# Kernel tuning notes

Measured on AMD Instinct MI355X. Metric: run time of the kernel, lower is better.

The kernel has to match this reference:

```python
import jax, jax.numpy as jnp
import numpy as np


def setup_inputs() -> dict:
    key = jax.random.key(0)
    k1, k2, k3 = jax.random.split(key, 3)
    B, C, H, W = 64, 512, 28, 28
    K = 32
    std = 1.0 / (K * C) ** 0.5
    x = jax.random.normal(k1, (B, C, H, W), dtype=jnp.float32)
    codewords = jax.random.uniform(k2, (K, C), dtype=jnp.float32, minval=-std, maxval=std)
    scale = jax.random.uniform(k3, (K,), dtype=jnp.float32, minval=-1.0, maxval=0.0)
    return {"x": x, "codewords": codewords, "scale": scale}


def reference(x, codewords, scale):
    # x: (B, C, H, W) -> descriptors (B, N, C)
    B, C, H, W = x.shape
    K = codewords.shape[0]
    xd = x.reshape(B, C, H * W).transpose(0, 2, 1)  # (B, N, C)

    # scaled L2: scale_k * ||x_n - c_k||^2, expanded without (B,N,K,C) intermediate
    x_sq = jnp.sum(xd * xd, axis=-1, keepdims=True)            # (B, N, 1)
    c_sq = jnp.sum(codewords * codewords, axis=-1)             # (K,)
    xc = jnp.einsum("bnc,kc->bnk", xd, codewords)              # (B, N, K)
    dist = scale * (x_sq - 2.0 * xc + c_sq)                    # (B, N, K)

    A = jax.nn.softmax(dist, axis=2)                           # (B, N, K)

    # encoded_k = sum_n A[b,n,k] * (x[b,n] - c[k])
    wx = jnp.einsum("bnk,bnc->bkc", A, xd)                     # (B, K, C)
    wsum = jnp.sum(A, axis=1)                                  # (B, K)
    encoded = wx - wsum[:, :, None] * codewords[None, :, :]    # (B, K, C)
    return encoded
```

## Files before the change

kernel.cpp:

```cpp
#include <hip/hip_runtime.h>

#define BB 64
#define CC 512
#define NPIX 784
#define KK 32
#define NSA 13
#define AS 800
#define CW_S 520
#define NSTEP 24

typedef __attribute__((ext_vector_type(8))) short short8;
typedef __attribute__((ext_vector_type(4))) float floatx4;
typedef __attribute__((ext_vector_type(4))) unsigned short ushort4v;

#define WSUM_OFF (BB * KK * AS)

__device__ __forceinline__ unsigned short f2bf(float f) {
    union { float f; unsigned u; } v; v.f = f;
    return (unsigned short)((v.u + 0x7FFFu + ((v.u >> 16) & 1u)) >> 16);
}
__device__ __forceinline__ float bf2f(unsigned short h) {
    union { unsigned u; float f; } v; v.u = ((unsigned)h) << 16; return v.f;
}
__device__ __forceinline__ short8 pack8(const float4& a, const float4& b) {
    short8 r;
    r[0] = (short)f2bf(a.x); r[1] = (short)f2bf(a.y);
    r[2] = (short)f2bf(a.z); r[3] = (short)f2bf(a.w);
    r[4] = (short)f2bf(b.x); r[5] = (short)f2bf(b.y);
    r[6] = (short)f2bf(b.z); r[7] = (short)f2bf(b.w);
    return r;
}

__global__ __launch_bounds__(256, 4) void kA(const float* __restrict__ x,
                                             const float* __restrict__ cw,
                                             const float* __restrict__ scale,
                                             unsigned short* __restrict__ Ag)
{
    __shared__ __align__(16) unsigned short cs[KK * CW_S];
    __shared__ float csq_p[8][KK];
    __shared__ float csq_l[KK];
    __shared__ float wredA[4][KK];

    const int t    = threadIdx.x;
    const int lane = t & 63, w = t >> 6;
    const int col  = lane & 15, quad = lane >> 4;
    const int split = blockIdx.x, b = blockIdx.y;
    const int p0    = (split < 12) ? split * 64 : 720;

    if (split == 0 && t < 64) {
        const short8 z = {0, 0, 0, 0, 0, 0, 0, 0};
        const int k = t >> 1, off = (t & 1) * 8;
        *(short8*)&Ag[(size_t)b * KK * AS + (size_t)k * AS + NPIX + off] = z;
    }

#pragma unroll 4
    for (int j = 0; j < 16; ++j) {
        const int qidx = t + j * 256;
        const int row = qidx >> 7, qc = qidx & 127;
        const float4 v = *(const float4*)&cw[row * CC + qc * 4];
        ushort4v p; p.x = f2bf(v.x); p.y = f2bf(v.y); p.z = f2bf(v.z); p.w = f2bf(v.w);
        *(ushort4v*)&cs[row * CW_S + qc * 4] = p;
    }
    __syncthreads();
    {
        const int k = t & 31, part = t >> 5;
        float s = 0.f;
        for (int i = 0; i < 64; ++i) {
            const float v = bf2f(cs[k * CW_S + part * 64 + i]);
            s += v * v;
        }
        csq_p[part][k] = s;
    }
    __syncthreads();
    if (t < KK) {
        float s = 0.f;
#pragma unroll
        for (int p = 0; p < 8; ++p) s += csq_p[p][t];
        csq_l[t] = s;
    }
    __syncthreads();

    const float s0 = scale[col], s1 = scale[col + 16];
    const float q0 = csq_l[col], q1 = csq_l[col + 16];

    const int px = p0 + w * 16 + col;
    const float* xb = x + (size_t)b * CC * NPIX + px;

    floatx4 acc0 = {0.f, 0.f, 0.f, 0.f};
    floatx4 acc1 = {0.f, 0.f, 0.f, 0.f};
    float xsqp = 0.f;
    float buf[3][8];

#pragma unroll
    for (int j = 0; j < 8; ++j) buf[0][j] = xb[(size_t)(0 * 32 + quad * 8 + j) * NPIX];
#pragma unroll
    for (int j = 0; j < 8; ++j) buf[1][j] = xb[(size_t)(1 * 32 + quad * 8 + j) * NPIX];

#pragma unroll
    for (int kc = 0; kc < 16; ++kc) {
        const int cur = kc % 3;
        if (kc + 2 < 16) {
            const int nb = (kc + 2) % 3;
            const int cb = (kc + 2) * 32 + quad * 8;
#pragma unroll
            for (int j = 0; j < 8; ++j) buf[nb][j] = xb[(size_t)(cb + j) * NPIX];
        }
        short8 a;
#pragma unroll
        for (int j = 0; j < 8; ++j) {
            const float v = buf[cur][j];
            xsqp += v * v;
            a[j] = (short)f2bf(v);
        }
        const int cb0 = kc * 32 + quad * 8;
        const short8 b0 = *(const short8*)&cs[col * CW_S + cb0];
        const short8 b1 = *(const short8*)&cs[(col + 16) * CW_S + cb0];
        acc0 = __builtin_amdgcn_mfma_f32_16x16x32_bf16(a, b0, acc0, 0, 0, 0);
        acc1 = __builtin_amdgcn_mfma_f32_16x16x32_bf16(a, b1, acc1, 0, 0, 0);
    }

    xsqp += __shfl_xor(xsqp, 16);
    xsqp += __shfl_xor(xsqp, 32);

    unsigned short* Ab = Ag + (size_t)b * KK * AS + p0 + w * 16;
    float ts0 = 0.f, ts1 = 0.f;
#pragma unroll
    for (int r = 0; r < 4; ++r) {
        const float xq = __shfl(xsqp, quad * 4 + r);
        const float d0 = s0 * (xq + q0 - 2.f * acc0[r]);
        const float d1 = s1 * (xq + q1 - 2.f * acc1[r]);
        float mx = fmaxf(d0, d1);
        mx = fmaxf(mx, __shfl_xor(mx, 1));
        mx = fmaxf(mx, __shfl_xor(mx, 2));
        mx = fmaxf(mx, __shfl_xor(mx, 4));
        mx = fmaxf(mx, __shfl_xor(mx, 8));
        const float e0 = __expf(d0 - mx), e1 = __expf(d1 - mx);
        float sm = e0 + e1;
        sm += __shfl_xor(sm, 1);
        sm += __shfl_xor(sm, 2);
        sm += __shfl_xor(sm, 4);
        sm += __shfl_xor(sm, 8);
        const float inv = 1.f / sm;
        const float a0 = e0 * inv, a1 = e1 * inv;
        Ab[col * AS + quad * 4 + r]        = f2bf(a0);
        Ab[(col + 16) * AS + quad * 4 + r] = f2bf(a1);
        ts0 += a0; ts1 += a1;
    }

    ts0 += __shfl_xor(ts0, 16); ts0 += __shfl_xor(ts0, 32);
    ts1 += __shfl_xor(ts1, 16); ts1 += __shfl_xor(ts1, 32);
    if (quad == 0) { wredA[w][col] = ts0; wredA[w][col + 16] = ts1; }
    __syncthreads();
    if (t < KK) {
        float s;
        if (split < 12) s = wredA[0][t] + wredA[1][t] + wredA[2][t] + wredA[3][t];
        else            s = wredA[3][t];
        float* wsf = (float*)(Ag + WSUM_OFF);
        wsf[(size_t)(split * BB + b) * KK + t] = s;
    }
}

__global__ __launch_bounds__(256) void kB(const float* __restrict__ x,
                                          const float* __restrict__ cw,
                                          const unsigned short* __restrict__ Ag,
                                          float* __restrict__ out)
{
    __shared__ float wsum_l[KK];

    const int t    = threadIdx.x;
    const int lane = t & 63, w = t >> 6;
    const int col  = lane & 15, quad = lane >> 4;
    const int cch  = blockIdx.x, b = blockIdx.y;

    const unsigned short* Ab = Ag + (size_t)b * KK * AS;

    if (t < KK) {
        const float* wsf = (const float*)(Ag + WSUM_OFF);
        float s = 0.f;
#pragma unroll
        for (int sp = 0; sp < NSA; ++sp) s += wsf[(size_t)(sp * BB + b) * KK + t];
        wsum_l[t] = s;
    }

    const int c = cch * 64 + w * 16 + col;
    const float* xp = x + ((size_t)b * CC + c) * NPIX;
    const unsigned short* a0p = Ab + (size_t)col * AS;
    const unsigned short* a1p = Ab + (size_t)(col + 16) * AS;
    const int qo = quad * 8;

    floatx4 acc0 = {0.f, 0.f, 0.f, 0.f};
    floatx4 acc1 = {0.f, 0.f, 0.f, 0.f};
#pragma unroll 6
    for (int s = 0; s < NSTEP; ++s) {
        const int off = s * 32 + qo;
        const short8 av0 = *(const short8*)&a0p[off];
        const short8 av1 = *(const short8*)&a1p[off];
        const float4 xv0 = *(const float4*)&xp[off];
        const float4 xv1 = *(const float4*)&xp[off + 4];
        const short8 bv = pack8(xv0, xv1);
        acc0 = __builtin_amdgcn_mfma_f32_16x16x32_bf16(av0, bv, acc0, 0, 0, 0);
        acc1 = __builtin_amdgcn_mfma_f32_16x16x32_bf16(av1, bv, acc1, 0, 0, 0);
    }
    {
        const int off = NSTEP * 32 + qo;
        const short8 av0 = *(const short8*)&a0p[off];
        const short8 av1 = *(const short8*)&a1p[off];
        float4 xv0 = make_float4(0.f, 0.f, 0.f, 0.f);
        float4 xv1 = make_float4(0.f, 0.f, 0.f, 0.f);
        if (quad < 2) {
            xv0 = *(const float4*)&xp[off];
            xv1 = *(const float4*)&xp[off + 4];
        }
        const short8 bv = pack8(xv0, xv1);
        acc0 = __builtin_amdgcn_mfma_f32_16x16x32_bf16(av0, bv, acc0, 0, 0, 0);
        acc1 = __builtin_amdgcn_mfma_f32_16x16x32_bf16(av1, bv, acc1, 0, 0, 0);
    }

    __syncthreads();

    float* ob = out + (size_t)b * KK * CC + c;
    const float* cp = cw + c;
#pragma unroll
    for (int r = 0; r < 4; ++r) {
        const int k0 = quad * 4 + r;
        ob[(size_t)k0 * CC]        = acc0[r] - wsum_l[k0]      * cp[(size_t)k0 * CC];
        ob[(size_t)(k0 + 16) * CC] = acc1[r] - wsum_l[k0 + 16] * cp[(size_t)(k0 + 16) * CC];
    }
}

extern "C" void kernel_launch(void* const* d_in, const int* in_sizes, int n_in,
                              void* d_out, int out_size, void* d_ws, size_t ws_size,
                              hipStream_t stream) {
    const float* x     = (const float*)d_in[0];
    const float* cw    = (const float*)d_in[1];
    const float* scale = (const float*)d_in[2];
    float* out = (float*)d_out;
    unsigned short* Ag = (unsigned short*)d_ws;

    kA<<<dim3(NSA, BB), dim3(256), 0, stream>>>(x, cw, scale, Ag);
    kB<<<dim3(8, BB), dim3(256), 0, stream>>>(x, cw, Ag, out);
}
```

Measured before the change: 183.4 us.

## Stream x tiles into LDS via global_load_lds double buffering in kA

Replaces the register triple-buffered x loads in kA with direct global-to-LDS asynchronous loads (global_load_lds), double-buffered per wave with explicit vmcnt waits, so more loads stay in flight while the MFMAs run. LDS use grows by 32 KB per block and launch_bounds occupancy drops from 4 to 2 blocks per CU. The intent is to hide global latency better. The cost is lower occupancy and manual waitcnt scheduling that depends on the exact count of outstanding loads.

```diff
diff --git a/kernel.cpp b/kernel.cpp
--- a/kernel.cpp
+++ b/kernel.cpp
@@ -31,12 +31,28 @@
     return r;
 }
 
-__global__ __launch_bounds__(256, 4) void kA(const float* __restrict__ x,
+#define GLOAD_LDS(gp, lp)                                                       \
+    __builtin_amdgcn_global_load_lds(                                           \
+        (const __attribute__((address_space(1))) unsigned int*)(const void*)(gp), \
+        (__attribute__((address_space(3))) unsigned int*)(void*)(lp), 4, 0, 0)
+
+#define ISSUEG(g, bf) {                                                         \
+    _Pragma("unroll")                                                           \
+    for (int _kl = 0; _kl < 2; ++_kl) {                                         \
+        _Pragma("unroll")                                                       \
+        for (int _j = 0; _j < 8; ++_j) {                                        \
+            const float* _src = xb + (size_t)((g) * 64 + _kl * 32 + quad * 8 + _j) * NPIX; \
+            GLOAD_LDS(_src, &gbuf[w][bf][(_kl * 8 + _j) * 64]);                 \
+        }                                                                       \
+    } }
+
+__global__ __launch_bounds__(256, 2) void kA(const float* __restrict__ x,
                                              const float* __restrict__ cw,
                                              const float* __restrict__ scale,
                                              unsigned short* __restrict__ Ag)
 {
     __shared__ __align__(16) unsigned short cs[KK * CW_S];
+    __shared__ __align__(16) float gbuf[4][2][1024];
     __shared__ float csq_p[8][KK];
     __shared__ float csq_l[KK];
     __shared__ float wredA[4][KK];
@@ -89,34 +105,32 @@
     floatx4 acc0 = {0.f, 0.f, 0.f, 0.f};
     floatx4 acc1 = {0.f, 0.f, 0.f, 0.f};
     float xsqp = 0.f;
-    float buf[3][8];
-
-#pragma unroll
-    for (int j = 0; j < 8; ++j) buf[0][j] = xb[(size_t)(0 * 32 + quad * 8 + j) * NPIX];
-#pragma unroll
-    for (int j = 0; j < 8; ++j) buf[1][j] = xb[(size_t)(1 * 32 + quad * 8 + j) * NPIX];
-
-#pragma unroll
-    for (int kc = 0; kc < 16; ++kc) {
-        const int cur = kc % 3;
-        if (kc + 2 < 16) {
-            const int nb = (kc + 2) % 3;
-            const int cb = (kc + 2) * 32 + quad * 8;
-#pragma unroll
-            for (int j = 0; j < 8; ++j) buf[nb][j] = xb[(size_t)(cb + j) * NPIX];
-        }
-        short8 a;
-#pragma unroll
-        for (int j = 0; j < 8; ++j) {
-            const float v = buf[cur][j];
-            xsqp += v * v;
-            a[j] = (short)f2bf(v);
-        }
-        const int cb0 = kc * 32 + quad * 8;
-        const short8 b0 = *(const short8*)&cs[col * CW_S + cb0];
-        const short8 b1 = *(const short8*)&cs[(col + 16) * CW_S + cb0];
-        acc0 = __builtin_amdgcn_mfma_f32_16x16x32_bf16(a, b0, acc0, 0, 0, 0);
-        acc1 = __builtin_amdgcn_mfma_f32_16x16x32_bf16(a, b1, acc1, 0, 0, 0);
+
+    ISSUEG(0, 0);
+#pragma unroll
+    for (int g = 0; g < 8; ++g) {
+        if (g < 7) {
+            ISSUEG(g + 1, (g + 1) & 1);
+            asm volatile("s_waitcnt vmcnt(16)" ::: "memory");
+        } else {
+            asm volatile("s_waitcnt vmcnt(0)" ::: "memory");
+        }
+        __builtin_amdgcn_sched_barrier(0);
+#pragma unroll
+        for (int kl = 0; kl < 2; ++kl) {
+            const int kc = g * 2 + kl;
+            float va[8];
+#pragma unroll
+            for (int j = 0; j < 8; ++j) va[j] = gbuf[w][g & 1][(kl * 8 + j) * 64 + lane];
+            short8 a;
+#pragma unroll
+            for (int j = 0; j < 8; ++j) { xsqp += va[j] * va[j]; a[j] = (short)f2bf(va[j]); }
+            const int cb = kc * 32 + quad * 8;
+            const short8 b0 = *(const short8*)&cs[col * CW_S + cb];
+            const short8 b1 = *(const short8*)&cs[(col + 16) * CW_S + cb];
+            acc0 = __builtin_amdgcn_mfma_f32_16x16x32_bf16(a, b0, acc0, 0, 0, 0);
+            acc1 = __builtin_amdgcn_mfma_f32_16x16x32_bf16(a, b1, acc1, 0, 0, 0);
+        }
     }
 
     xsqp += __shfl_xor(xsqp, 16);
```

After: 182.2 us. No clear change (-0.6%).

## Precompute bf16 codewords once and stage x tile in LDS for kA

Applied to the files above, without the earlier changes.

Adds a one-block prep kernel that converts codewords to bf16 and computes their squared norms once into workspace, so each kA block no longer redoes this. kA now loads its 64-pixel x tile with coalesced float4 reads into a padded bf16 LDS buffer, computes x squared norms there, and reads MFMA operands from LDS. Codeword operands come straight from global/L2. The cost is an extra kernel launch and a large LDS footprint (about 66KB), which lowers occupancy (launch bounds reduced to 2).

```diff
diff --git a/kernel.cpp b/kernel.cpp
--- a/kernel.cpp
+++ b/kernel.cpp
@@ -6,7 +6,7 @@
 #define KK 32
 #define NSA 13
 #define AS 800
-#define CW_S 520
+#define XS_S 66
 #define NSTEP 24
 
 typedef __attribute__((ext_vector_type(8))) short short8;
@@ -14,13 +14,12 @@
 typedef __attribute__((ext_vector_type(4))) unsigned short ushort4v;
 
 #define WSUM_OFF (BB * KK * AS)
+#define CWB_OFF  (WSUM_OFF + 2 * NSA * BB * KK)
+#define CSQ_OFF  (CWB_OFF + KK * CC)
 
 __device__ __forceinline__ unsigned short f2bf(float f) {
     union { float f; unsigned u; } v; v.f = f;
     return (unsigned short)((v.u + 0x7FFFu + ((v.u >> 16) & 1u)) >> 16);
-}
-__device__ __forceinline__ float bf2f(unsigned short h) {
-    union { unsigned u; float f; } v; v.u = ((unsigned)h) << 16; return v.f;
 }
 __device__ __forceinline__ short8 pack8(const float4& a, const float4& b) {
     short8 r;
@@ -31,14 +30,39 @@
     return r;
 }
 
-__global__ __launch_bounds__(256, 4) void kA(const float* __restrict__ x,
-                                             const float* __restrict__ cw,
+__global__ __launch_bounds__(256) void kPrep(const float* __restrict__ cw,
+                                             unsigned short* __restrict__ Ag)
+{
+    __shared__ float red[KK][8];
+    const int t = threadIdx.x;
+    const int k = t >> 3, part = t & 7;
+    unsigned short* cwb = Ag + CWB_OFF;
+    float* csqg = (float*)(Ag + CSQ_OFF);
+    const float* cp = cw + k * CC + part * 64;
+    float s = 0.f;
+#pragma unroll 16
+    for (int i = 0; i < 64; ++i) {
+        const float v = cp[i];
+        s += v * v;
+        cwb[k * CC + part * 64 + i] = f2bf(v);
+    }
+    red[k][part] = s;
+    __syncthreads();
+    if (t < KK) {
+        float ss = 0.f;
+#pragma unroll
+        for (int p = 0; p < 8; ++p) ss += red[t][p];
+        csqg[t] = ss;
+    }
+}
+
+__global__ __launch_bounds__(256, 2) void kA(const float* __restrict__ x,
                                              const float* __restrict__ scale,
                                              unsigned short* __restrict__ Ag)
 {
-    __shared__ __align__(16) unsigned short cs[KK * CW_S];
-    __shared__ float csq_p[8][KK];
-    __shared__ float csq_l[KK];
+    __shared__ __align__(16) unsigned short xs[CC * XS_S];
+    __shared__ float xsq_p[16][64];
+    __shared__ float xsq_l[64];
     __shared__ float wredA[4][KK];
 
     const int t    = threadIdx.x;
@@ -53,80 +77,66 @@
         *(short8*)&Ag[(size_t)b * KK * AS + (size_t)k * AS + NPIX + off] = z;
     }
 
-#pragma unroll 4
-    for (int j = 0; j < 16; ++j) {
-        const int qidx = t + j * 256;
-        const int row = qidx >> 7, qc = qidx & 127;
-        const float4 v = *(const float4*)&cw[row * CC + qc * 4];
-        ushort4v p; p.x = f2bf(v.x); p.y = f2bf(v.y); p.z = f2bf(v.z); p.w = f2bf(v.w);
-        *(ushort4v*)&cs[row * CW_S + qc * 4] = p;
-    }
-    __syncthreads();
-    {
-        const int k = t & 31, part = t >> 5;
+    const float* xb = x + (size_t)b * CC * NPIX + p0;
+    const int csub = t >> 4;
+    const int pg   = t & 15;
+    float sx0 = 0.f, sx1 = 0.f, sx2 = 0.f, sx3 = 0.f;
+#pragma unroll
+    for (int g = 0; g < 4; ++g) {
+        float4 v[8];
+#pragma unroll
+        for (int i = 0; i < 8; ++i) {
+            const int c = (g * 8 + i) * 16 + csub;
+            v[i] = *(const float4*)&xb[(size_t)c * NPIX + pg * 4];
+        }
+#pragma unroll
+        for (int i = 0; i < 8; ++i) {
+            const int c = (g * 8 + i) * 16 + csub;
+            sx0 += v[i].x * v[i].x; sx1 += v[i].y * v[i].y;
+            sx2 += v[i].z * v[i].z; sx3 += v[i].w * v[i].w;
+            ushort4v p; p.x = f2bf(v[i].x); p.y = f2bf(v[i].y);
+            p.z = f2bf(v[i].z); p.w = f2bf(v[i].w);
+            *(ushort4v*)&xs[c * XS_S + pg * 4] = p;
+        }
+    }
+    xsq_p[csub][pg * 4 + 0] = sx0;
+    xsq_p[csub][pg * 4 + 1] = sx1;
+    xsq_p[csub][pg * 4 + 2] = sx2;
+    xsq_p[csub][pg * 4 + 3] = sx3;
+    __syncthreads();
+    if (t < 64) {
         float s = 0.f;
-        for (int i = 0; i < 64; ++i) {
-            const float v = bf2f(cs[k * CW_S + part * 64 + i]);
-            s += v * v;
-        }
-        csq_p[part][k] = s;
-    }
-    __syncthreads();
-    if (t < KK) {
-        float s = 0.f;
-#pragma unroll
-        for (int p = 0; p < 8; ++p) s += csq_p[p][t];
-        csq_l[t] = s;
-    }
-    __syncthreads();
-
+#pragma unroll
+        for (int r = 0; r < 16; ++r) s += xsq_p[r][t];
+        xsq_l[t] = s;
+    }
+    __syncthreads();
+
+    const unsigned short* cwb = Ag + CWB_OFF;
+    const float* csqg = (const float*)(Ag + CSQ_OFF);
     const float s0 = scale[col], s1 = scale[col + 16];
-    const float q0 = csq_l[col], q1 = csq_l[col + 16];
-
-    const int px = p0 + w * 16 + col;
-    const float* xb = x + (size_t)b * CC * NPIX + px;
+    const float q0 = csqg[col], q1 = csqg[col + 16];
+    const int wpx = w * 16 + col;
 
     floatx4 acc0 = {0.f, 0.f, 0.f, 0.f};
     floatx4 acc1 = {0.f, 0.f, 0.f, 0.f};
-    float xsqp = 0.f;
-    float buf[3][8];
-
-#pragma unroll
-    for (int j = 0; j < 8; ++j) buf[0][j] = xb[(size_t)(0 * 32 + quad * 8 + j) * NPIX];
-#pragma unroll
-    for (int j = 0; j < 8; ++j) buf[1][j] = xb[(size_t)(1 * 32 + quad * 8 + j) * NPIX];
-
 #pragma unroll
     for (int kc = 0; kc < 16; ++kc) {
-        const int cur = kc % 3;
-        if (kc + 2 < 16) {
-            const int nb = (kc + 2) % 3;
-            const int cb = (kc + 2) * 32 + quad * 8;
-#pragma unroll
-            for (int j = 0; j < 8; ++j) buf[nb][j] = xb[(size_t)(cb + j) * NPIX];
-        }
+        const int cb = kc * 32 + quad * 8;
         short8 a;
 #pragma unroll
-        for (int j = 0; j < 8; ++j) {
-            const float v = buf[cur][j];
-            xsqp += v * v;
-            a[j] = (short)f2bf(v);
-        }
-        const int cb0 = kc * 32 + quad * 8;
-        const short8 b0 = *(const short8*)&cs[col * CW_S + cb0];
-        const short8 b1 = *(const short8*)&cs[(col + 16) * CW_S + cb0];
+        for (int j = 0; j < 8; ++j) a[j] = (short)xs[(cb + j) * XS_S + wpx];
+        const short8 b0 = *(const short8*)&cwb[col * CC + cb];
+        const short8 b1 = *(const short8*)&cwb[(col + 16) * CC + cb];
         acc0 = __builtin_amdgcn_mfma_f32_16x16x32_bf16(a, b0, acc0, 0, 0, 0);
         acc1 = __builtin_amdgcn_mfma_f32_16x16x32_bf16(a, b1, acc1, 0, 0, 0);
     }
 
-    xsqp += __shfl_xor(xsqp, 16);
-    xsqp += __shfl_xor(xsqp, 32);
-
     unsigned short* Ab = Ag + (size_t)b * KK * AS + p0 + w * 16;
     float ts0 = 0.f, ts1 = 0.f;
 #pragma unroll
     for (int r = 0; r < 4; ++r) {
-        const float xq = __shfl(xsqp, quad * 4 + r);
+        const float xq = xsq_l[w * 16 + quad * 4 + r];
         const float d0 = s0 * (xq + q0 - 2.f * acc0[r]);
         const float d1 = s1 * (xq + q1 - 2.f * acc1[r]);
         float mx = fmaxf(d0, d1);
@@ -237,6 +247,7 @@
     float* out = (float*)d_out;
     unsigned short* Ag = (unsigned short*)d_ws;
 
-    kA<<<dim3(NSA, BB), dim3(256), 0, stream>>>(x, cw, scale, Ag);
+    kPrep<<<dim3(1), dim3(256), 0, stream>>>(cw, Ag);
+    kA<<<dim3(NSA, BB), dim3(256), 0, stream>>>(x, scale, Ag);
     kB<<<dim3(8, BB), dim3(256), 0, stream>>>(x, cw, Ag, out);
 }
```

New measurement: 196.1 us. 7.0% more time.
